# Kernel tuning notes

Measured on AMD Instinct MI355X. Metric: run time of the kernel, lower is better.

Reference implementation:

```python
import jax, jax.numpy as jnp
import numpy as np

N_SPARSE = 2  # keep N of every M weights (2:4 structured sparsity)
M_SPARSE = 4


def compute_mask(w, n, m):
    # w: [out, in]; zero the (m - n) smallest-|w| entries in each group of m
    out_f, in_f = w.shape
    k = m - n
    wr = jnp.abs(w).reshape(out_f, in_f // m, m)
    # indices of the k smallest |w| per group (torch.topk largest=False)
    _, idx = jax.lax.top_k(-wr, k)                      # [out, in/m, k]
    pruned = jax.nn.one_hot(idx, m, dtype=w.dtype).sum(axis=-2)  # [out, in/m, m]
    mask = 1.0 - pruned
    return mask.reshape(out_f, in_f)


def setup_inputs() -> dict:
    key = jax.random.key(0)
    k1, k2, k3 = jax.random.split(key, 3)
    B, S, Din, Dout = 64, 197, 768, 3072
    x = jax.random.normal(k1, (B, S, Din), dtype=jnp.float32)
    weight = jax.random.normal(k2, (Dout, Din), dtype=jnp.float32)
    bias = jax.random.normal(k3, (Dout,), dtype=jnp.float32)
    return {"x": x, "weight": weight, "bias": bias}


def reference(x, weight, bias):
    # mask is a precomputed buffer in torch (not differentiated)
    mask = compute_mask(jax.lax.stop_gradient(weight), N_SPARSE, M_SPARSE)
    w = weight * mask
    # F.linear: x @ w.T + b
    return jnp.einsum('bsi,oi->bso', x, w) + bias
```

## Files before the change

### kernel.cpp

```cpp
#include <hip/hip_runtime.h>
#include <hip/hip_bf16.h>

#define M_DIM 12608
#define K_DIM 768
#define N_DIM 3072
#define M_PAD 12800
#define BM 128
#define BN 256
#define BK 32
#define NT (K_DIM / BK)
#define MBLK (M_PAD / BM)
#define NBLK (N_DIM / BN)
#define NWG (MBLK * NBLK)

typedef __attribute__((ext_vector_type(8))) short bf16x8;
typedef __attribute__((ext_vector_type(4))) float f32x4;

__device__ __forceinline__ void gload_lds16(const void* g, void* l) {
  __builtin_amdgcn_global_load_lds(
      (const __attribute__((address_space(1))) unsigned int*)g,
      (__attribute__((address_space(3))) unsigned int*)l,
      16, 0, 0);
}

#define GX 4800
#define GW 2304
__global__ void cvt_fused(const float* __restrict__ x, const float* __restrict__ w,
                          __hip_bfloat16* __restrict__ xb, __hip_bfloat16* __restrict__ wb) {
  if (blockIdx.x < GX) {
    size_t i = ((size_t)blockIdx.x * 256 + threadIdx.x) * 8;
    union { __hip_bfloat16 h[8]; uint4 u; } o;
    if (i < (size_t)M_DIM * K_DIM) {
      float4 a = *(const float4*)(x + i);
      float4 b = *(const float4*)(x + i + 4);
      o.h[0] = __float2bfloat16(a.x); o.h[1] = __float2bfloat16(a.y);
      o.h[2] = __float2bfloat16(a.z); o.h[3] = __float2bfloat16(a.w);
      o.h[4] = __float2bfloat16(b.x); o.h[5] = __float2bfloat16(b.y);
      o.h[6] = __float2bfloat16(b.z); o.h[7] = __float2bfloat16(b.w);
    } else {
      o.u = make_uint4(0, 0, 0, 0);
    }
    *(uint4*)(xb + i) = o.u;
  } else {
    size_t g = ((size_t)(blockIdx.x - GX) * 256 + threadIdx.x);
    float4 v = *(const float4*)(w + g * 4);
    float val[4] = {v.x, v.y, v.z, v.w};
    float a[4] = {fabsf(v.x), fabsf(v.y), fabsf(v.z), fabsf(v.w)};
    union { __hip_bfloat16 h[4]; uint2 u; } o;
#pragma unroll
    for (int i = 0; i < 4; ++i) {
      int rank = 0;
#pragma unroll
      for (int j = 0; j < 4; ++j)
        rank += (a[j] > a[i]) || (a[j] == a[i] && j > i);
      o.h[i] = __float2bfloat16(rank < 2 ? val[i] : 0.0f);
    }
    *(uint2*)(wb + g * 4) = o.u;
  }
}

__global__ __launch_bounds__(256, 2) void gemm_bt(
    const __hip_bfloat16* __restrict__ A,
    const __hip_bfloat16* __restrict__ B,
    const float* __restrict__ bias,
    float* __restrict__ C)
{
  extern __shared__ char smem[];

  const int tid  = threadIdx.x;
  const int lane = tid & 63;
  const int wave = tid >> 6;
  const int wm   = wave >> 1;
  const int wn   = wave & 1;

  const int wg  = blockIdx.x;
  const int swz = (wg & 7) * (NWG / 8) + (wg >> 3);
  const int tile_m = (swz % MBLK) * BM;
  const int tile_n = (swz / MBLK) * BN;

  const int r2 = lane >> 2;
  const int p  = lane & 3;
  const int gsw = p ^ ((r2 >> 1) & 3);
  const __hip_bfloat16* asrc[2];
  const __hip_bfloat16* bsrc[4];
#pragma unroll
  for (int u = 0; u < 2; ++u)
    asrc[u] = A + (size_t)(tile_m + wave * 32 + u * 16 + r2) * K_DIM + gsw * 8;
#pragma unroll
  for (int u = 0; u < 4; ++u)
    bsrc[u] = B + (size_t)(tile_n + wave * 64 + u * 16 + r2) * K_DIM + gsw * 8;

  const int frow  = lane & 15;
  const int fslot = (lane >> 4) ^ ((frow >> 1) & 3);
  const int abase = (wm * 64 + frow) * 64 + fslot * 16;
  const int bbase = 8192 + (wn * 128 + frow) * 64 + fslot * 16;

  f32x4 acc[4][8] = {};

#pragma unroll
  for (int u = 0; u < 2; ++u)
    gload_lds16(asrc[u], smem + (wave * 2 + u) * 1024);
#pragma unroll
  for (int u = 0; u < 4; ++u)
    gload_lds16(bsrc[u], smem + 8192 + (wave * 4 + u) * 1024);
#pragma unroll
  for (int u = 0; u < 2; ++u)
    gload_lds16(asrc[u] + BK, smem + 24576 + (wave * 2 + u) * 1024);
#pragma unroll
  for (int u = 0; u < 4; ++u)
    gload_lds16(bsrc[u] + BK, smem + 24576 + 8192 + (wave * 4 + u) * 1024);

#pragma unroll 3
  for (int t = 0; t < NT; ++t) {
    if (t < NT - 1) { asm volatile("s_waitcnt vmcnt(6)" ::: "memory"); }
    else            { asm volatile("s_waitcnt vmcnt(0)" ::: "memory"); }
    __builtin_amdgcn_s_barrier();

    if (t + 2 < NT) {
      char* nb = smem + ((t + 2) % 3) * 24576;
      const int off = (t + 2) * BK;
#pragma unroll
      for (int u = 0; u < 2; ++u)
        gload_lds16(asrc[u] + off, nb + (wave * 2 + u) * 1024);
#pragma unroll
      for (int u = 0; u < 4; ++u)
        gload_lds16(bsrc[u] + off, nb + 8192 + (wave * 4 + u) * 1024);
    }

    const char* bq = smem + (t % 3) * 24576;
    bf16x8 af[4], bfv[8];
#pragma unroll
    for (int m = 0; m < 4; ++m)
      af[m] = *(const bf16x8*)(bq + abase + m * 1024);
#pragma unroll
    for (int n = 0; n < 8; ++n)
      bfv[n] = *(const bf16x8*)(bq + bbase + n * 1024);
    __builtin_amdgcn_s_setprio(1);
#pragma unroll
    for (int m = 0; m < 4; ++m)
#pragma unroll
      for (int n = 0; n < 8; ++n)
        acc[m][n] = __builtin_amdgcn_mfma_f32_16x16x32_bf16(af[m], bfv[n], acc[m][n], 0, 0, 0);
    __builtin_amdgcn_s_setprio(0);
  }

  const int ccol = lane & 15;
  const int quad = lane >> 4;
  float bv[8];
#pragma unroll
  for (int n = 0; n < 8; ++n)
    bv[n] = bias[tile_n + wn * 128 + n * 16 + ccol];

#pragma unroll
  for (int m = 0; m < 4; ++m) {
    const int rbase = tile_m + wm * 64 + m * 16 + quad * 4;
#pragma unroll
    for (int r = 0; r < 4; ++r) {
      const int grow = rbase + r;
      if (grow < M_DIM) {
        float* crow = C + (size_t)grow * N_DIM + tile_n + wn * 128;
#pragma unroll
        for (int n = 0; n < 8; ++n)
          crow[n * 16 + ccol] = acc[m][n][r] + bv[n];
      }
    }
  }
}

extern "C" void kernel_launch(void* const* d_in, const int* in_sizes, int n_in,
                              void* d_out, int out_size, void* d_ws, size_t ws_size,
                              hipStream_t stream) {
  const float* x    = (const float*)d_in[0];
  const float* w    = (const float*)d_in[1];
  const float* bias = (const float*)d_in[2];
  float* out = (float*)d_out;

  __hip_bfloat16* xb = (__hip_bfloat16*)d_ws;
  __hip_bfloat16* wb = xb + (size_t)M_PAD * K_DIM;

  static bool attr_set = false;
  if (!attr_set) {
    hipFuncSetAttribute(reinterpret_cast<const void*>(gemm_bt),
                        hipFuncAttributeMaxDynamicSharedMemorySize, 73728);
    attr_set = true;
  }

  cvt_fused<<<GX + GW, 256, 0, stream>>>(x, w, xb, wb);
  gemm_bt<<<NWG, 256, 73728, stream>>>(xb, wb, bias, out);
}
```

Before: 265.3 us.

## Switch GEMM to 256x128 tiles with 8 waves and 32x32x16 MFMA

Reshapes the GEMM block tile from 128x256 to 256x128 and doubles the block to 512 threads (8 waves, 4x2 layout, 64x64 output per wave). It replaces the 16x16x32 bf16 MFMA with 32x32x16 bf16 MFMA, and rewrites the LDS fragment offsets, the global-to-LDS load mapping and the epilogue row mapping to match. The goal is fewer LDS fragment reads per MFMA and more waves resident to hide latency. The trade-off is the launch bound of (512, 4), which may squeeze the per-thread register budget enough to cause accumulator spills.

```diff
diff --git a/kernel.cpp b/kernel.cpp
--- a/kernel.cpp
+++ b/kernel.cpp
@@ -5,8 +5,8 @@
 #define K_DIM 768
 #define N_DIM 3072
 #define M_PAD 12800
-#define BM 128
-#define BN 256
+#define BM 256
+#define BN 128
 #define BK 32
 #define NT (K_DIM / BK)
 #define MBLK (M_PAD / BM)
@@ -14,7 +14,7 @@
 #define NWG (MBLK * NBLK)
 
 typedef __attribute__((ext_vector_type(8))) short bf16x8;
-typedef __attribute__((ext_vector_type(4))) float f32x4;
+typedef __attribute__((ext_vector_type(16))) float f32x16;
 
 __device__ __forceinline__ void gload_lds16(const void* g, void* l) {
   __builtin_amdgcn_global_load_lds(
@@ -59,7 +59,7 @@
   }
 }
 
-__global__ __launch_bounds__(256, 2) void gemm_bt(
+__global__ __launch_bounds__(512, 4) void gemm_bt(
     const __hip_bfloat16* __restrict__ A,
     const __hip_bfloat16* __restrict__ B,
     const float* __restrict__ bias,
@@ -75,93 +75,93 @@
 
   const int wg  = blockIdx.x;
   const int swz = (wg & 7) * (NWG / 8) + (wg >> 3);
-  const int tile_m = (swz % MBLK) * BM;
-  const int tile_n = (swz / MBLK) * BN;
+  const int tile_m = (swz / NBLK) * BM;
+  const int tile_n = (swz % NBLK) * BN;
 
-  const int r2 = lane >> 2;
-  const int p  = lane & 3;
-  const int gsw = p ^ ((r2 >> 1) & 3);
-  const __hip_bfloat16* asrc[2];
-  const __hip_bfloat16* bsrc[4];
+  const int l4 = lane >> 2;
+  const int gk = ((lane & 3) ^ ((lane >> 3) & 3)) * 8;
+  const __hip_bfloat16* ag = A + (size_t)(tile_m + wave * 16 + l4) * K_DIM + gk;
+  const __hip_bfloat16* bg = B + (size_t)(tile_n + wave * 16 + l4) * K_DIM + gk;
+
+  const int half = lane >> 5;
+  const int lrow = lane & 31;
+  const int arow0 = wm * 64 + lrow;
+  const int brow0 = wn * 64 + lrow;
+  const int af_ = (arow0 >> 1) & 3;
+  const int bf_ = (brow0 >> 1) & 3;
+  int aoff[2][2], boff[2][2];
 #pragma unroll
-  for (int u = 0; u < 2; ++u)
-    asrc[u] = A + (size_t)(tile_m + wave * 32 + u * 16 + r2) * K_DIM + gsw * 8;
+  for (int j = 0; j < 2; ++j)
 #pragma unroll
-  for (int u = 0; u < 4; ++u)
-    bsrc[u] = B + (size_t)(tile_n + wave * 64 + u * 16 + r2) * K_DIM + gsw * 8;
+    for (int s = 0; s < 2; ++s) {
+      aoff[j][s] = (arow0 + s * 32) * 64 + (((j * 2 + half) ^ af_) << 4);
+      boff[j][s] = 16384 + (brow0 + s * 32) * 64 + (((j * 2 + half) ^ bf_) << 4);
+    }
 
-  const int frow  = lane & 15;
-  const int fslot = (lane >> 4) ^ ((frow >> 1) & 3);
-  const int abase = (wm * 64 + frow) * 64 + fslot * 16;
-  const int bbase = 8192 + (wn * 128 + frow) * 64 + fslot * 16;
+  f32x16 acc[2][2] = {};
 
-  f32x4 acc[4][8] = {};
-
-#pragma unroll
-  for (int u = 0; u < 2; ++u)
-    gload_lds16(asrc[u], smem + (wave * 2 + u) * 1024);
-#pragma unroll
-  for (int u = 0; u < 4; ++u)
-    gload_lds16(bsrc[u], smem + 8192 + (wave * 4 + u) * 1024);
-#pragma unroll
-  for (int u = 0; u < 2; ++u)
-    gload_lds16(asrc[u] + BK, smem + 24576 + (wave * 2 + u) * 1024);
-#pragma unroll
-  for (int u = 0; u < 4; ++u)
-    gload_lds16(bsrc[u] + BK, smem + 24576 + 8192 + (wave * 4 + u) * 1024);
+  {
+    char* b0 = smem;
+    gload_lds16(ag, b0 + wave * 1024);
+    gload_lds16(ag + (size_t)128 * K_DIM, b0 + 8192 + wave * 1024);
+    gload_lds16(bg, b0 + 16384 + wave * 1024);
+    char* b1 = smem + 24576;
+    gload_lds16(ag + BK, b1 + wave * 1024);
+    gload_lds16(ag + (size_t)128 * K_DIM + BK, b1 + 8192 + wave * 1024);
+    gload_lds16(bg + BK, b1 + 16384 + wave * 1024);
+  }
 
 #pragma unroll 3
   for (int t = 0; t < NT; ++t) {
-    if (t < NT - 1) { asm volatile("s_waitcnt vmcnt(6)" ::: "memory"); }
+    if (t < NT - 1) { asm volatile("s_waitcnt vmcnt(3)" ::: "memory"); }
     else            { asm volatile("s_waitcnt vmcnt(0)" ::: "memory"); }
     __builtin_amdgcn_s_barrier();
 
     if (t + 2 < NT) {
       char* nb = smem + ((t + 2) % 3) * 24576;
-      const int off = (t + 2) * BK;
-#pragma unroll
-      for (int u = 0; u < 2; ++u)
-        gload_lds16(asrc[u] + off, nb + (wave * 2 + u) * 1024);
-#pragma unroll
-      for (int u = 0; u < 4; ++u)
-        gload_lds16(bsrc[u] + off, nb + 8192 + (wave * 4 + u) * 1024);
+      const size_t off = (size_t)(t + 2) * BK;
+      gload_lds16(ag + off, nb + wave * 1024);
+      gload_lds16(ag + (size_t)128 * K_DIM + off, nb + 8192 + wave * 1024);
+      gload_lds16(bg + off, nb + 16384 + wave * 1024);
     }
 
     const char* bq = smem + (t % 3) * 24576;
-    bf16x8 af[4], bfv[8];
+    bf16x8 afr[2][2], bfr[2][2];
 #pragma unroll
-    for (int m = 0; m < 4; ++m)
-      af[m] = *(const bf16x8*)(bq + abase + m * 1024);
+    for (int j = 0; j < 2; ++j)
 #pragma unroll
-    for (int n = 0; n < 8; ++n)
-      bfv[n] = *(const bf16x8*)(bq + bbase + n * 1024);
+      for (int s = 0; s < 2; ++s) {
+        afr[j][s] = *(const bf16x8*)(bq + aoff[j][s]);
+        bfr[j][s] = *(const bf16x8*)(bq + boff[j][s]);
+      }
     __builtin_amdgcn_s_setprio(1);
 #pragma unroll
-    for (int m = 0; m < 4; ++m)
+    for (int mi = 0; mi < 2; ++mi)
 #pragma unroll
-      for (int n = 0; n < 8; ++n)
-        acc[m][n] = __builtin_amdgcn_mfma_f32_16x16x32_bf16(af[m], bfv[n], acc[m][n], 0, 0, 0);
+      for (int ni = 0; ni < 2; ++ni) {
+        acc[mi][ni] = __builtin_amdgcn_mfma_f32_32x32x16_bf16(afr[0][mi], bfr[0][ni], acc[mi][ni], 0, 0, 0);
+        acc[mi][ni] = __builtin_amdgcn_mfma_f32_32x32x16_bf16(afr[1][mi], bfr[1][ni], acc[mi][ni], 0, 0, 0);
+      }
     __builtin_amdgcn_s_setprio(0);
   }
 
-  const int ccol = lane & 15;
-  const int quad = lane >> 4;
-  float bv[8];
+  const int ccol = lane & 31;
+  float bv[2];
 #pragma unroll
-  for (int n = 0; n < 8; ++n)
-    bv[n] = bias[tile_n + wn * 128 + n * 16 + ccol];
+  for (int ni = 0; ni < 2; ++ni)
+    bv[ni] = bias[tile_n + wn * 64 + ni * 32 + ccol];
 
 #pragma unroll
-  for (int m = 0; m < 4; ++m) {
-    const int rbase = tile_m + wm * 64 + m * 16 + quad * 4;
+  for (int mi = 0; mi < 2; ++mi) {
+    const int rb = tile_m + wm * 64 + mi * 32 + half * 4;
 #pragma unroll
-    for (int r = 0; r < 4; ++r) {
-      const int grow = rbase + r;
-      if (grow < M_DIM) {
-        float* crow = C + (size_t)grow * N_DIM + tile_n + wn * 128;
+    for (int ni = 0; ni < 2; ++ni) {
+      float* cp = C + (size_t)0 * N_DIM + tile_n + wn * 64 + ni * 32 + ccol;
 #pragma unroll
-        for (int n = 0; n < 8; ++n)
-          crow[n * 16 + ccol] = acc[m][n][r] + bv[n];
+      for (int reg = 0; reg < 16; ++reg) {
+        const int grow = rb + (reg & 3) + 8 * (reg >> 2);
+        if (grow < M_DIM)
+          cp[(size_t)grow * N_DIM] = acc[mi][ni][reg] + bv[ni];
       }
     }
   }
@@ -186,5 +186,5 @@
   }
 
   cvt_fused<<<GX + GW, 256, 0, stream>>>(x, w, xb, wb);
-  gemm_bt<<<NWG, 256, 73728, stream>>>(xb, wb, bias, out);
+  gemm_bt<<<NWG, 512, 73728, stream>>>(xb, wb, bias, out);
 }
```

After: 252.2 us. 4.9% less time.
